# Performance work log

Measured on AMD Instinct MI355X. Metric: run time of the kernel, lower is better.

## Reference

```python
import jax, jax.numpy as jnp
import numpy as np


def setup_inputs() -> dict:
    key = jax.random.key(0)
    kx, ke = jax.random.split(key)
    B, D, H, W, K = 64, 64, 32, 32, 512
    x = jax.random.normal(kx, (B, D, H, W), dtype=jnp.float32)
    # matches nn.init.normal_(weight, mean=0.0, std=2*D**-0.5)
    emb = jax.random.normal(ke, (D, K), dtype=jnp.float32) * (2.0 * D ** -0.5)
    return {"x": x, "emb": emb}


def reference(x, emb):
    # x: (B, D, *spatial), emb: (D, K)
    B, D = x.shape[0], x.shape[1]
    spatial = x.shape[2:]
    xf = jnp.moveaxis(x, 1, -1).reshape(B, -1, D)  # (B, N, D)
    scores = -2.0 * jnp.einsum('bnd,dk->bnk', xf, emb) + jnp.sum(emb * emb, axis=0)  # (B, N, K)
    argmin = jnp.argmin(scores, axis=-1)  # (B, N) int
    quant = jnp.take(emb.T, argmin, axis=0)  # (B, N, D) gather from codebook
    result = jnp.moveaxis(quant.reshape(B, *spatial, D), -1, 1)  # (B, D, *spatial)
    return result, argmin.reshape(B, *spatial)
```

## Files before the change

### kernel.cpp

```cpp
#include <hip/hip_runtime.h>


constexpr int D  = 64;
constexpr int K  = 512;
constexpr int HW = 1024;

__global__ __launch_bounds__(512, 4) void vq_argmin_kernel(
    const float* __restrict__ x,
    const float* __restrict__ emb,
    float* __restrict__ out_q,
    float* __restrict__ out_idx)
{
    __shared__ float e2s[K];
    __shared__ float mb[3][128];
    __shared__ int   mi[3][128];
    __shared__ int   kfin[128];

    const int tid   = threadIdx.x;
    const int rl    = tid & 127;
    const int slice = __builtin_amdgcn_readfirstlane(tid >> 7);
    const int r     = blockIdx.x * 128 + rl;
    const int b     = r >> 10;
    const int n     = r & 1023;

    {
        float s = 0.f;
        #pragma unroll 16
        for (int d = 0; d < D; ++d) {
            float v = emb[d * K + tid];
            s = fmaf(v, v, s);
        }
        e2s[tid] = s;
    }

    const float* xr = x + (size_t)(b * D) * HW + n;
    float xv[D];
    #pragma unroll
    for (int d = 0; d < D; ++d) xv[d] = xr[(size_t)d * HW];

    __syncthreads();

    float best = 3.4e38f;
    int   bidx = 0;
    const int kbase = slice * 128;

    for (int g = 0; g < 8; ++g) {
        const int k0 = kbase + g * 16;
        const float* ep = emb + k0;
        float acc[16];
        #pragma unroll
        for (int i = 0; i < 16; ++i) acc[i] = 0.f;

        #pragma unroll
        for (int d = 0; d < D; ++d) {
            const float xd = xv[d];
            #pragma unroll
            for (int i = 0; i < 16; ++i)
                acc[i] = fmaf(xd, ep[d * K + i], acc[i]);
        }

        #pragma unroll
        for (int i = 0; i < 16; ++i) {
            float s = fmaf(-2.f, acc[i], e2s[k0 + i]);
            if (s < best) { best = s; bidx = k0 + i; }
        }
    }

    if (slice > 0) { mb[slice - 1][rl] = best; mi[slice - 1][rl] = bidx; }
    __syncthreads();

    if (tid < 128) {
        #pragma unroll
        for (int s = 0; s < 3; ++s) {
            float ob = mb[s][tid];
            int   oi = mi[s][tid];
            if (ob < best) { best = ob; bidx = oi; }
        }
        kfin[tid] = bidx;
        __builtin_nontemporal_store((float)bidx, &out_idx[blockIdx.x * 128 + tid]);
    }
    __syncthreads();

    const int kq = kfin[rl];
    float* oq = out_q + (size_t)(b * D) * HW + n;
    #pragma unroll
    for (int j = 0; j < 16; ++j) {
        int d = slice * 16 + j;
        __builtin_nontemporal_store(emb[d * K + kq], &oq[(size_t)d * HW]);
    }
}

extern "C" void kernel_launch(void* const* d_in, const int* in_sizes, int n_in,
                              void* d_out, int out_size, void* d_ws, size_t ws_size,
                              hipStream_t stream)
{
    const float* x   = (const float*)d_in[0];
    const float* emb = (const float*)d_in[1];

    float* out_q   = (float*)d_out;
    float* out_idx = out_q + (size_t)64 * 64 * 1024;

    vq_argmin_kernel<<<512, 512, 0, stream>>>(x, emb, out_q, out_idx);
}
```

Measured before the change: 142.4 us.

## Tile distance GEMM through LDS with 4x8 register blocking per thread

Replaces the per-thread row-in-registers scheme, where each thread streamed codebook values from global memory, with an LDS-tiled GEMM. Each 256-thread block stages 64 rows of x and 128-column codebook chunks in shared memory, and each thread computes a 4x8 tile of scores. The per-row argmin is then reduced with wave shuffles and a lowest-index tie-break. This is meant to cut redundant global or L2 codebook traffic and raise the ratio of FMAs to loads. The cost is more LDS use, extra barriers per chunk, and a different launch shape (1024 blocks of 256 threads).

```diff
diff --git a/kernel.cpp b/kernel.cpp
--- a/kernel.cpp
+++ b/kernel.cpp
@@ -1,91 +1,139 @@
 #include <hip/hip_runtime.h>
 
 
-constexpr int D  = 64;
-constexpr int K  = 512;
-constexpr int HW = 1024;
+constexpr int D    = 64;
+constexpr int K    = 512;
+constexpr int HW   = 1024;
+constexpr int ROWS = 64;
+constexpr int CK   = 128;
+constexpr int NCH  = K / CK;
 
-__global__ __launch_bounds__(512, 4) void vq_argmin_kernel(
+__global__ __launch_bounds__(256, 3) void vq_kernel(
     const float* __restrict__ x,
     const float* __restrict__ emb,
     float* __restrict__ out_q,
     float* __restrict__ out_idx)
 {
+    __shared__ float xs[D][ROWS];
+    __shared__ float es[D][CK];
     __shared__ float e2s[K];
-    __shared__ float mb[3][128];
-    __shared__ int   mi[3][128];
-    __shared__ int   kfin[128];
+    __shared__ int   kfin[ROWS];
 
-    const int tid   = threadIdx.x;
-    const int rl    = tid & 127;
-    const int slice = __builtin_amdgcn_readfirstlane(tid >> 7);
-    const int r     = blockIdx.x * 128 + rl;
-    const int b     = r >> 10;
-    const int n     = r & 1023;
+    const int tid = threadIdx.x;
+    const int ct  = tid & 15;
+    const int rg  = tid >> 4;
+    const int r0  = blockIdx.x * ROWS;
+    const int b   = r0 >> 10;
+    const int n0  = r0 & (HW - 1);
 
-    {
+    const float* xg = x + ((size_t)b * D) * HW + n0;
+
+    #pragma unroll
+    for (int h = 0; h < 2; ++h) {
+        const int k = h * 256 + tid;
         float s = 0.f;
-        #pragma unroll 16
+        #pragma unroll
         for (int d = 0; d < D; ++d) {
-            float v = emb[d * K + tid];
+            const float v = emb[d * K + k];
             s = fmaf(v, v, s);
         }
-        e2s[tid] = s;
+        e2s[k] = s;
     }
 
-    const float* xr = x + (size_t)(b * D) * HW + n;
-    float xv[D];
     #pragma unroll
-    for (int d = 0; d < D; ++d) xv[d] = xr[(size_t)d * HW];
+    for (int p = 0; p < 4; ++p) {
+        const int li = p * 256 + tid;
+        const int d  = li >> 4;
+        const int r4 = (li & 15) << 2;
+        const float4 v = *reinterpret_cast<const float4*>(xg + (size_t)d * HW + r4);
+        *reinterpret_cast<float4*>(&xs[d][r4]) = v;
+    }
 
-    __syncthreads();
+    float best[4] = {3.4e38f, 3.4e38f, 3.4e38f, 3.4e38f};
+    int   bidx[4] = {0, 0, 0, 0};
 
-    float best = 3.4e38f;
-    int   bidx = 0;
-    const int kbase = slice * 128;
+    for (int ch = 0; ch < NCH; ++ch) {
+        __syncthreads();
 
-    for (int g = 0; g < 8; ++g) {
-        const int k0 = kbase + g * 16;
-        const float* ep = emb + k0;
-        float acc[16];
         #pragma unroll
-        for (int i = 0; i < 16; ++i) acc[i] = 0.f;
+        for (int p = 0; p < 8; ++p) {
+            const int li = p * 256 + tid;
+            const int d  = li >> 5;
+            const int c4 = (li & 31) << 2;
+            const float4 v = *reinterpret_cast<const float4*>(emb + d * K + ch * CK + c4);
+            *reinterpret_cast<float4*>(&es[d][c4]) = v;
+        }
+        __syncthreads();
+
+        float acc[4][8];
+        #pragma unroll
+        for (int j = 0; j < 4; ++j)
+            #pragma unroll
+            for (int i = 0; i < 8; ++i) acc[j][i] = 0.f;
 
         #pragma unroll
         for (int d = 0; d < D; ++d) {
-            const float xd = xv[d];
+            const float4 xv  = *reinterpret_cast<const float4*>(&xs[d][rg << 2]);
+            const float4 ev0 = *reinterpret_cast<const float4*>(&es[d][ct << 3]);
+            const float4 ev1 = *reinterpret_cast<const float4*>(&es[d][(ct << 3) + 4]);
+            const float* xf  = reinterpret_cast<const float*>(&xv);
+            const float* ef0 = reinterpret_cast<const float*>(&ev0);
+            const float* ef1 = reinterpret_cast<const float*>(&ev1);
             #pragma unroll
-            for (int i = 0; i < 16; ++i)
-                acc[i] = fmaf(xd, ep[d * K + i], acc[i]);
+            for (int j = 0; j < 4; ++j) {
+                const float xj = xf[j];
+                #pragma unroll
+                for (int i = 0; i < 4; ++i) {
+                    acc[j][i]     = fmaf(xj, ef0[i], acc[j][i]);
+                    acc[j][i + 4] = fmaf(xj, ef1[i], acc[j][i + 4]);
+                }
+            }
         }
 
+        const int kb = ch * CK + (ct << 3);
+        const float4 q0 = *reinterpret_cast<const float4*>(&e2s[kb]);
+        const float4 q1 = *reinterpret_cast<const float4*>(&e2s[kb + 4]);
+        const float* qf0 = reinterpret_cast<const float*>(&q0);
+        const float* qf1 = reinterpret_cast<const float*>(&q1);
         #pragma unroll
-        for (int i = 0; i < 16; ++i) {
-            float s = fmaf(-2.f, acc[i], e2s[k0 + i]);
-            if (s < best) { best = s; bidx = k0 + i; }
+        for (int j = 0; j < 4; ++j) {
+            #pragma unroll
+            for (int i = 0; i < 8; ++i) {
+                const float e2 = (i < 4) ? qf0[i] : qf1[i - 4];
+                const float s  = fmaf(-2.f, acc[j][i], e2);
+                if (s < best[j]) { best[j] = s; bidx[j] = kb + i; }
+            }
         }
     }
 
-    if (slice > 0) { mb[slice - 1][rl] = best; mi[slice - 1][rl] = bidx; }
-    __syncthreads();
+    #pragma unroll
+    for (int m = 1; m < 16; m <<= 1) {
+        #pragma unroll
+        for (int j = 0; j < 4; ++j) {
+            const float ob = __shfl_xor(best[j], m, 64);
+            const int   oi = __shfl_xor(bidx[j], m, 64);
+            if (ob < best[j] || (ob == best[j] && oi < bidx[j])) {
+                best[j] = ob; bidx[j] = oi;
+            }
+        }
+    }
 
-    if (tid < 128) {
+    if (ct == 0) {
         #pragma unroll
-        for (int s = 0; s < 3; ++s) {
-            float ob = mb[s][tid];
-            int   oi = mi[s][tid];
-            if (ob < best) { best = ob; bidx = oi; }
+        for (int j = 0; j < 4; ++j) {
+            kfin[(rg << 2) + j] = bidx[j];
+            __builtin_nontemporal_store((float)bidx[j], &out_idx[r0 + (rg << 2) + j]);
         }
-        kfin[tid] = bidx;
-        __builtin_nontemporal_store((float)bidx, &out_idx[blockIdx.x * 128 + tid]);
     }
     __syncthreads();
 
-    const int kq = kfin[rl];
-    float* oq = out_q + (size_t)(b * D) * HW + n;
+    const int row = tid & 63;
+    const int dg  = tid >> 6;
+    const int kq  = kfin[row];
+    float* oq = out_q + ((size_t)b * D) * HW + n0 + row;
     #pragma unroll
     for (int j = 0; j < 16; ++j) {
-        int d = slice * 16 + j;
+        const int d = (dg << 4) + j;
         __builtin_nontemporal_store(emb[d * K + kq], &oq[(size_t)d * HW]);
     }
 }
@@ -100,5 +148,5 @@
     float* out_q   = (float*)d_out;
     float* out_idx = out_q + (size_t)64 * 64 * 1024;
 
-    vq_argmin_kernel<<<512, 512, 0, stream>>>(x, emb, out_q, out_idx);
+    vq_kernel<<<1024, 256, 0, stream>>>(x, emb, out_q, out_idx);
 }
```

Result: faster. 127.7 us (-10.3%).
